# Kernel optimization log

Measured on AMD Instinct MI355X. Metric: run time of the kernel, lower is better.

## Reference

```python
import jax, jax.numpy as jnp
import numpy as np

NUM_HEADS = 8
NEG_INF = float(-2**32 + 1)
LN_EPS = 1e-8


def setup_inputs() -> dict:
    key = jax.random.key(0)
    ks = jax.random.split(key, 9)
    B, T, D = 4, 2048, 512
    inp = {
        "queries": jax.random.normal(ks[0], (B, T, D), jnp.float32),
        "keys": jax.random.normal(ks[1], (B, T, D), jnp.float32),
        "values": jax.random.normal(ks[2], (B, T, D), jnp.float32),
        "Wq": jax.random.normal(ks[3], (D, D), jnp.float32) / np.sqrt(D),
        "bq": jnp.zeros((D,), jnp.float32),
        "Wk": jax.random.normal(ks[4], (D, D), jnp.float32) / np.sqrt(D),
        "bk": jnp.zeros((D,), jnp.float32),
        "Wv": jax.random.normal(ks[5], (D, D), jnp.float32) / np.sqrt(D),
        "bv": jnp.zeros((D,), jnp.float32),
        "gamma": jnp.ones((D,), jnp.float32),
        "beta": jnp.zeros((D,), jnp.float32),
    }
    return inp


def _split_heads(x, h):
    # torch.cat(torch.chunk(x, h, dim=2), dim=0): [B,T,D] -> [h*B, T, D/h], head-major
    B, T, D = x.shape
    return x.reshape(B, T, h, D // h).transpose(2, 0, 1, 3).reshape(h * B, T, D // h)


def _merge_heads(x, h, B):
    # inverse: [h*B, T, dh] -> [B, T, h*dh]
    hB, T, dh = x.shape
    return x.reshape(h, B, T, dh).transpose(1, 2, 0, 3).reshape(B, T, h * dh)


def reference(queries, keys, values, Wq, bq, Wk, bk, Wv, bv, gamma, beta):
    h = NUM_HEADS
    B, Tq, D = queries.shape
    dh = D // h

    Q = jax.nn.relu(queries @ Wq + bq)
    K = jax.nn.relu(keys @ Wk + bk)
    V = jax.nn.relu(values @ Wv + bv)

    Q_ = _split_heads(Q, h)  # [h*B, Tq, dh]
    K_ = _split_heads(K, h)
    V_ = _split_heads(V, h)

    scores = jnp.einsum('bqd,bkd->bqk', Q_, K_) / jnp.sqrt(jnp.float32(dh))  # [h*B, Tq, Tk]

    # key padding mask: zero rows in `keys` get -inf scores
    key_mask = jnp.sign(jnp.abs(jnp.sum(keys, axis=-1)))  # [B, Tk]
    key_mask = jnp.tile(key_mask, (h, 1))  # [h*B, Tk]
    scores = jnp.where(key_mask[:, None, :] == 0.0, NEG_INF, scores)

    attn = jax.nn.softmax(scores, axis=-1)

    # query mask applied multiplicatively post-softmax
    query_mask = jnp.sign(jnp.abs(jnp.sum(queries, axis=-1)))  # [B, Tq]
    query_mask = jnp.tile(query_mask, (h, 1))  # [h*B, Tq]
    attn = attn * query_mask[:, :, None]

    out = jnp.einsum('bqk,bkd->bqd', attn, V_)  # [h*B, Tq, dh]
    out = _merge_heads(out, h, B) + queries  # residual

    # custom LayerNorm: torch.std is unbiased (ddof=1), eps added to std
    mean = out.mean(-1, keepdims=True)
    std = jnp.sqrt(out.var(-1, ddof=1, keepdims=True))
    return gamma * (out - mean) / (std + LN_EPS) + beta
```

## Files before the change

### kernel.cpp

```cpp
#include <hip/hip_runtime.h>


typedef __attribute__((ext_vector_type(8))) __bf16 bf16x8;
typedef __attribute__((ext_vector_type(4))) float f32x4;

#if __has_builtin(__builtin_amdgcn_exp2f)
#define EXP2F __builtin_amdgcn_exp2f
#else
#define EXP2F exp2f
#endif

#define QSCALE (0.125f * 1.4426950408889634f)

__device__ __forceinline__ unsigned short f2bf(float f) {
  return __builtin_bit_cast(unsigned short, (__bf16)f);
}
__device__ __forceinline__ unsigned pk2(float a, float b) {
  return (unsigned)f2bf(a) | ((unsigned)f2bf(b) << 16);
}
__device__ __forceinline__ f32x4 mfma16(bf16x8 a, bf16x8 b, f32x4 c) {
  return __builtin_amdgcn_mfma_f32_16x16x32_bf16(a, b, c, 0, 0, 0);
}
__device__ __forceinline__ bf16x8 ld_bf8(const unsigned short* p) {
  return *(const bf16x8*)p;
}
__device__ __forceinline__ void g2l16(const void* g, void* l) {
  __builtin_amdgcn_global_load_lds(
      (const __attribute__((address_space(1))) void*)g,
      (__attribute__((address_space(3))) void*)l, 16, 0, 0);
}

__global__ __launch_bounds__(256) void wt_kernel(const float* __restrict__ Wq,
                                                 const float* __restrict__ Wk,
                                                 const float* __restrict__ Wv,
                                                 unsigned short* __restrict__ Wt) {
  int idx = blockIdx.x * 256 + threadIdx.x;
  int o = idx * 8;
  int z = o >> 18;
  int rem = o & 262143;
  int n = rem >> 9;
  int k0 = rem & 511;
  const float* W = (z == 0) ? Wq : ((z == 1) ? Wk : Wv);
  unsigned int w[4];
#pragma unroll
  for (int i = 0; i < 4; ++i) {
    unsigned short lo = f2bf(W[(k0 + 2 * i) * 512 + n]);
    unsigned short hi = f2bf(W[(k0 + 2 * i + 1) * 512 + n]);
    w[i] = (unsigned)lo | ((unsigned)hi << 16);
  }
  *(uint4*)(Wt + o) = make_uint4(w[0], w[1], w[2], w[3]);
}

__global__ __launch_bounds__(256) void xcvt_kernel(
    const float* __restrict__ Xq, const float* __restrict__ Xk,
    const float* __restrict__ Xv, unsigned short* __restrict__ Xbq,
    unsigned short* __restrict__ Xbk, unsigned short* __restrict__ Xbv,
    float* __restrict__ qmask, float* __restrict__ kbias) {
  int row = blockIdx.x * 4 + (threadIdx.x >> 6);
  int lane = threadIdx.x & 63;
  int z = row >> 13;
  int r = row & 8191;
  const float* X = (z == 0) ? Xq : ((z == 1) ? Xk : Xv);
  unsigned short* Xb = (z == 0) ? Xbq : ((z == 1) ? Xbk : Xbv);
  const float* p = X + r * 512 + lane * 8;
  f32x4 lo = *(const f32x4*)p;
  f32x4 hi = *(const f32x4*)(p + 4);
  *(uint4*)(Xb + r * 512 + lane * 8) =
      make_uint4(pk2(lo[0], lo[1]), pk2(lo[2], lo[3]), pk2(hi[0], hi[1]),
                 pk2(hi[2], hi[3]));
  if (z < 2) {
    float s = lo[0] + lo[1] + lo[2] + lo[3] + hi[0] + hi[1] + hi[2] + hi[3];
#pragma unroll
    for (int off = 1; off < 64; off <<= 1) s += __shfl_xor(s, off);
    if (lane == 0) {
      if (z == 0)
        qmask[r] = (s == 0.f) ? 0.f : 1.f;
      else
        kbias[r] = (s == 0.f) ? -1.0e30f : 0.f;
    }
  }
}

__global__ __launch_bounds__(256, 3) void proj_kernel(
    const unsigned short* __restrict__ Xbq, const unsigned short* __restrict__ Xbk,
    const unsigned short* __restrict__ Xbv, const float* __restrict__ bq,
    const float* __restrict__ bk, const float* __restrict__ bv,
    const unsigned short* __restrict__ Wt, unsigned short* __restrict__ Qb,
    unsigned short* __restrict__ Kb, unsigned short* __restrict__ Vt) {
  __shared__ unsigned short Asm[2][128][32];
  __shared__ unsigned short Bsm[2][128][32];

  int tid = threadIdx.x;
  int m0g = blockIdx.x * 128;
  int z = m0g >> 13;
  int m0 = m0g & 8191;
  int n0 = blockIdx.y * 128;
  const unsigned short* Xb = (z == 0) ? Xbq : ((z == 1) ? Xbk : Xbv);
  const float* bias = (z == 0) ? bq : ((z == 1) ? bk : bv);
  const unsigned short* Wz = Wt + z * 262144;

  int w = tid >> 6, lane = tid & 63;
  int wm = w >> 1, wn = w & 1;
  int mrow = lane & 15, quad = lane >> 4;

  int srow = tid >> 2, sslot = tid & 3;
  int sxs = sslot ^ ((srow >> 1) & 3);
  const unsigned short* gA = Xb + (m0 + srow) * 512 + sxs * 8;
  const unsigned short* gB = Wz + (n0 + srow) * 512 + sxs * 8;
  char* lA = (char*)&Asm[0][0][0] + tid * 16;
  char* lB = (char*)&Bsm[0][0][0] + tid * 16;

  int rs = (quad ^ ((mrow >> 1) & 3)) * 8;

  f32x4 zero = {0.f, 0.f, 0.f, 0.f};
  f32x4 acc[4][4];
#pragma unroll
  for (int i = 0; i < 4; ++i)
#pragma unroll
    for (int j = 0; j < 4; ++j) acc[i][j] = zero;

  g2l16(gA, lA);
  g2l16(gA + 64 * 512, lA + 4096);
  g2l16(gB, lB);
  g2l16(gB + 64 * 512, lB + 4096);
  __syncthreads();

  for (int kc = 0; kc < 16; ++kc) {
    int cur = kc & 1;
    if (kc < 15) {
      int ko = (kc + 1) * 32;
      int nb = cur ^ 1;
      g2l16(gA + ko, lA + nb * 8192);
      g2l16(gA + ko + 64 * 512, lA + nb * 8192 + 4096);
      g2l16(gB + ko, lB + nb * 8192);
      g2l16(gB + ko + 64 * 512, lB + nb * 8192 + 4096);
    }
    bf16x8 af[4], bfr[4];
#pragma unroll
    for (int mt = 0; mt < 4; ++mt)
      af[mt] = ld_bf8(&Asm[cur][wm * 64 + mt * 16 + mrow][rs]);
#pragma unroll
    for (int nt = 0; nt < 4; ++nt)
      bfr[nt] = ld_bf8(&Bsm[cur][wn * 64 + nt * 16 + mrow][rs]);
#pragma unroll
    for (int mt = 0; mt < 4; ++mt)
#pragma unroll
      for (int nt = 0; nt < 4; ++nt)
        acc[mt][nt] = mfma16(af[mt], bfr[nt], acc[mt][nt]);
    __syncthreads();
  }

  if (z < 2) {
    unsigned short* dst = (z == 0) ? Qb : Kb;
    float sc = (z == 0) ? QSCALE : 1.0f;
#pragma unroll
    for (int nt = 0; nt < 4; ++nt) {
      int n = n0 + wn * 64 + nt * 16 + mrow;
      float bv_ = bias[n];
#pragma unroll
      for (int mt = 0; mt < 4; ++mt) {
        int m = m0 + wm * 64 + mt * 16 + quad * 4;
#pragma unroll
        for (int r = 0; r < 4; ++r) {
          float v = fmaxf(acc[mt][nt][r] + bv_, 0.f) * sc;
          dst[(m + r) * 512 + n] = f2bf(v);
        }
      }
    }
  } else {
#pragma unroll
    for (int nt = 0; nt < 4; ++nt) {
      int n = n0 + wn * 64 + nt * 16 + mrow;
      int hh = n >> 6, jj = n & 63;
      float bv_ = bias[n];
#pragma unroll
      for (int mt = 0; mt < 4; ++mt) {
        int grow = m0 + wm * 64 + mt * 16 + quad * 4;
        int bb = grow >> 11, tl = grow & 2047;
        int pos = (tl & ~31) + quad * 8 + (mt & 1) * 4;
        float p0 = fmaxf(acc[mt][nt][0] + bv_, 0.f);
        float p1 = fmaxf(acc[mt][nt][1] + bv_, 0.f);
        float p2 = fmaxf(acc[mt][nt][2] + bv_, 0.f);
        float p3 = fmaxf(acc[mt][nt][3] + bv_, 0.f);
        *(uint2*)(Vt + ((hh * 4 + bb) * 64 + jj) * 2048 + pos) =
            make_uint2(pk2(p0, p1), pk2(p2, p3));
      }
    }
  }
}

__global__ __launch_bounds__(256, 2) void attn_kernel(
    const unsigned short* __restrict__ Qb, const unsigned short* __restrict__ Kb,
    const unsigned short* __restrict__ Vt, const float* __restrict__ qmask,
    const float* __restrict__ kbias, const float* __restrict__ queries,
    float* __restrict__ out) {
  __shared__ char smem[65536];
  unsigned short* KsmS = (unsigned short*)smem;
  unsigned short* VsmS = (unsigned short*)(smem + 32768);

  int hb = blockIdx.x;
  int qt = blockIdx.y;
  int h = hb >> 2, b = hb & 3;
  int q0 = qt * 128;
  int tid = threadIdx.x;
  int w = tid >> 6, lane = tid & 63;
  int mrow = lane & 15, quad = lane >> 4;
  int mlow = mrow & 7;

  const unsigned short* gK =
      Kb + (b * 2048 + (tid >> 3)) * 512 + h * 64 + (((tid & 7) ^ ((tid >> 3) & 7)) * 8);
  const unsigned short* gV =
      Vt + (hb * 64 + (tid >> 4)) * 2048 + (((tid & 15) ^ ((tid >> 4) & 15)) * 8);

  bf16x8 qf[2][2];
  {
    const unsigned short* qp =
        Qb + (b * 2048 + q0 + w * 32 + mrow) * 512 + h * 64 + quad * 8;
#pragma unroll
    for (int qn = 0; qn < 2; ++qn) {
      qf[qn][0] = ld_bf8(qp + qn * 8192);
      qf[qn][1] = ld_bf8(qp + qn * 8192 + 32);
    }
  }

  bf16x8 onev;
#pragma unroll
  for (int i = 0; i < 8; ++i) onev[i] = (__bf16)1.0f;

  f32x4 zero = {0.f, 0.f, 0.f, 0.f};
  f32x4 oacc[4][2];
#pragma unroll
  for (int i = 0; i < 4; ++i)
#pragma unroll
    for (int j = 0; j < 2; ++j) oacc[i][j] = zero;
  f32x4 lacc[2] = {zero, zero};

  const float* kmB = kbias + b * 2048 + quad * 4;

#pragma unroll
  for (int j = 0; j < 4; ++j) {
    g2l16(gK + j * 32 * 512, &KsmS[j * 2048 + tid * 8]);
    g2l16(gV + j * 16 * 2048, &VsmS[j * 2048 + tid * 8]);
  }

  for (int it = 0; it < 16; ++it) {
    int bi = it & 1;
    int kb = it * 128;
    __syncthreads();

    if (it < 15) {
      int nb = 1 - bi;
      int nkb = kb + 128;
#pragma unroll
      for (int j = 0; j < 4; ++j) {
        g2l16(gK + (nkb + j * 32) * 512, &KsmS[nb * 8192 + j * 2048 + tid * 8]);
        g2l16(gV + nkb + j * 16 * 2048, &VsmS[nb * 8192 + j * 2048 + tid * 8]);
      }
    }

    const unsigned short* Kc = KsmS + bi * 8192;
    const unsigned short* Vc = VsmS + bi * 8192;

    bf16x8 kf[2][4], vf[2][4];
    f32x4 km[2][2];
    auto ldg = [&](int gi, int sl) {
      km[sl][0] = *(const f32x4*)(kmB + kb + gi * 32);
      km[sl][1] = *(const f32x4*)(kmB + kb + gi * 32 + 16);
      kf[sl][0] = ld_bf8(&Kc[(gi * 32 + mrow) * 64 + (quad ^ mlow) * 8]);
      kf[sl][1] = ld_bf8(&Kc[(gi * 32 + mrow) * 64 + ((4 + quad) ^ mlow) * 8]);
      kf[sl][2] = ld_bf8(&Kc[(gi * 32 + 16 + mrow) * 64 + (quad ^ mlow) * 8]);
      kf[sl][3] = ld_bf8(&Kc[(gi * 32 + 16 + mrow) * 64 + ((4 + quad) ^ mlow) * 8]);
#pragma unroll
      for (int dt = 0; dt < 4; ++dt)
        vf[sl][dt] =
            ld_bf8(&Vc[(dt * 16 + mrow) * 128 + ((gi * 4 + quad) ^ mrow) * 8]);
    };

    ldg(0, 0);
#pragma unroll
    for (int g = 0; g < 4; ++g) {
      int cb = g & 1;
      if (g < 3) ldg(g + 1, cb ^ 1);
#pragma unroll
      for (int qn = 0; qn < 2; ++qn) {
        f32x4 s0 = mfma16(kf[cb][0], qf[qn][0], km[cb][0]);
        s0 = mfma16(kf[cb][1], qf[qn][1], s0);
        f32x4 s1 = mfma16(kf[cb][2], qf[qn][0], km[cb][1]);
        s1 = mfma16(kf[cb][3], qf[qn][1], s1);
        f32x4 p0, p1;
#pragma unroll
        for (int r = 0; r < 4; ++r) {
          p0[r] = EXP2F(s0[r]);
          p1[r] = EXP2F(s1[r]);
        }
        bf16x8 pf = __builtin_bit_cast(
            bf16x8, make_uint4(pk2(p0[0], p0[1]), pk2(p0[2], p0[3]),
                               pk2(p1[0], p1[1]), pk2(p1[2], p1[3])));
        lacc[qn] = mfma16(pf, onev, lacc[qn]);
#pragma unroll
        for (int dt = 0; dt < 4; ++dt)
          oacc[dt][qn] = mfma16(pf, vf[cb][dt], oacc[dt][qn]);
      }
    }
  }

#pragma unroll
  for (int qn = 0; qn < 2; ++qn) {
#pragma unroll
    for (int r = 0; r < 4; ++r) {
      int qg = b * 2048 + q0 + w * 32 + qn * 16 + quad * 4 + r;
      float inv = qmask[qg] / lacc[qn][r];
      const float* qsrc = queries + qg * 512 + h * 64 + mrow;
      float* od = out + qg * 512 + h * 64 + mrow;
#pragma unroll
      for (int dt = 0; dt < 4; ++dt)
        od[dt * 16] = oacc[dt][qn][r] * inv + qsrc[dt * 16];
    }
  }
}

__global__ __launch_bounds__(256) void ln_kernel(float* __restrict__ out,
                                                 const float* __restrict__ gamma,
                                                 const float* __restrict__ beta) {
  int row = blockIdx.x * 4 + (threadIdx.x >> 6);
  int lane = threadIdx.x & 63;
  float* p = out + row * 512;
  float4 v1 = ((const float4*)p)[lane];
  float4 v2 = ((const float4*)p)[64 + lane];
  float s = v1.x + v1.y + v1.z + v1.w + v2.x + v2.y + v2.z + v2.w;
  float sq = v1.x * v1.x + v1.y * v1.y + v1.z * v1.z + v1.w * v1.w +
             v2.x * v2.x + v2.y * v2.y + v2.z * v2.z + v2.w * v2.w;
#pragma unroll
  for (int off = 32; off > 0; off >>= 1) {
    s += __shfl_xor(s, off);
    sq += __shfl_xor(sq, off);
  }
  float mean = s * (1.f / 512.f);
  float var = fmaxf((sq - 512.f * mean * mean) * (1.f / 511.f), 0.f);
  float inv = 1.f / (sqrtf(var) + 1e-8f);
  float4 g1 = ((const float4*)gamma)[lane];
  float4 g2 = ((const float4*)gamma)[64 + lane];
  float4 b1 = ((const float4*)beta)[lane];
  float4 b2 = ((const float4*)beta)[64 + lane];
  v1.x = g1.x * (v1.x - mean) * inv + b1.x;
  v1.y = g1.y * (v1.y - mean) * inv + b1.y;
  v1.z = g1.z * (v1.z - mean) * inv + b1.z;
  v1.w = g1.w * (v1.w - mean) * inv + b1.w;
  v2.x = g2.x * (v2.x - mean) * inv + b2.x;
  v2.y = g2.y * (v2.y - mean) * inv + b2.y;
  v2.z = g2.z * (v2.z - mean) * inv + b2.z;
  v2.w = g2.w * (v2.w - mean) * inv + b2.w;
  ((float4*)p)[lane] = v1;
  ((float4*)p)[64 + lane] = v2;
}

extern "C" void kernel_launch(void* const* d_in, const int* in_sizes, int n_in,
                              void* d_out, int out_size, void* d_ws, size_t ws_size,
                              hipStream_t stream) {
  (void)in_sizes; (void)n_in; (void)out_size; (void)ws_size;
  const float* queries = (const float*)d_in[0];
  const float* keys    = (const float*)d_in[1];
  const float* values  = (const float*)d_in[2];
  const float* Wq = (const float*)d_in[3];
  const float* bq = (const float*)d_in[4];
  const float* Wk = (const float*)d_in[5];
  const float* bk = (const float*)d_in[6];
  const float* Wv = (const float*)d_in[7];
  const float* bv = (const float*)d_in[8];
  const float* gamma = (const float*)d_in[9];
  const float* beta  = (const float*)d_in[10];
  float* out = (float*)d_out;

  char* ws = (char*)d_ws;
  unsigned short* Qb = (unsigned short*)(ws);
  unsigned short* Kb = (unsigned short*)(ws + 8 * 1024 * 1024);
  unsigned short* Vt = (unsigned short*)(ws + 16 * 1024 * 1024);
  unsigned short* Wt = (unsigned short*)(ws + 24 * 1024 * 1024);
  unsigned short* Xbv = (unsigned short*)(ws + 26 * 1024 * 1024);
  float* qmask = (float*)(ws + 34 * 1024 * 1024);
  float* kbias = qmask + 8192;

  unsigned short* Xbq = (unsigned short*)d_out;
  unsigned short* Xbk = Xbq + 4194304;

  wt_kernel<<<384, 256, 0, stream>>>(Wq, Wk, Wv, Wt);
  xcvt_kernel<<<6144, 256, 0, stream>>>(queries, keys, values, Xbq, Xbk, Xbv,
                                        qmask, kbias);
  proj_kernel<<<dim3(192, 4), 256, 0, stream>>>(Xbq, Xbk, Xbv, bq, bk, bv,
                                                Wt, Qb, Kb, Vt);
  attn_kernel<<<dim3(32, 16), 256, 0, stream>>>(Qb, Kb, Vt, qmask, kbias,
                                                queries, out);
  ln_kernel<<<2048, 256, 0, stream>>>(out, gamma, beta);
}
```

Measured before the change: 187.2 us.

## Split attention over the key dimension and merge partial sums in the layernorm kernel

```diff
diff --git a/kernel.cpp b/kernel.cpp
--- a/kernel.cpp
+++ b/kernel.cpp
@@ -189,38 +189,38 @@
   }
 }
 
-__global__ __launch_bounds__(256, 2) void attn_kernel(
+__global__ __launch_bounds__(256, 4) void attn_kernel(
     const unsigned short* __restrict__ Qb, const unsigned short* __restrict__ Kb,
-    const unsigned short* __restrict__ Vt, const float* __restrict__ qmask,
-    const float* __restrict__ kbias, const float* __restrict__ queries,
-    float* __restrict__ out) {
-  __shared__ char smem[65536];
+    const unsigned short* __restrict__ Vt, const float* __restrict__ kbias,
+    float* __restrict__ O0, float* __restrict__ O1,
+    float* __restrict__ l0, float* __restrict__ l1) {
+  __shared__ char smem[32768];
   unsigned short* KsmS = (unsigned short*)smem;
-  unsigned short* VsmS = (unsigned short*)(smem + 32768);
 
   int hb = blockIdx.x;
   int qt = blockIdx.y;
+  int z = blockIdx.z;
   int h = hb >> 2, b = hb & 3;
   int q0 = qt * 128;
+  int k0 = z * 1024;
   int tid = threadIdx.x;
   int w = tid >> 6, lane = tid & 63;
   int mrow = lane & 15, quad = lane >> 4;
   int mlow = mrow & 7;
 
   const unsigned short* gK =
-      Kb + (b * 2048 + (tid >> 3)) * 512 + h * 64 + (((tid & 7) ^ ((tid >> 3) & 7)) * 8);
-  const unsigned short* gV =
-      Vt + (hb * 64 + (tid >> 4)) * 2048 + (((tid & 15) ^ ((tid >> 4) & 15)) * 8);
+      Kb + (b * 2048 + k0 + (tid >> 3)) * 512 + h * 64 +
+      (((tid & 7) ^ ((tid >> 3) & 7)) * 8);
+  const unsigned short* gVb = Vt + (hb * 64 + mrow) * 2048 + k0;
 
   bf16x8 qf[2][2];
   {
     const unsigned short* qp =
         Qb + (b * 2048 + q0 + w * 32 + mrow) * 512 + h * 64 + quad * 8;
-#pragma unroll
-    for (int qn = 0; qn < 2; ++qn) {
-      qf[qn][0] = ld_bf8(qp + qn * 8192);
-      qf[qn][1] = ld_bf8(qp + qn * 8192 + 32);
-    }
+    qf[0][0] = ld_bf8(qp);
+    qf[0][1] = ld_bf8(qp + 32);
+    qf[1][0] = ld_bf8(qp + 8192);
+    qf[1][1] = ld_bf8(qp + 8192 + 32);
   }
 
   bf16x8 onev;
@@ -235,45 +235,38 @@
     for (int j = 0; j < 2; ++j) oacc[i][j] = zero;
   f32x4 lacc[2] = {zero, zero};
 
-  const float* kmB = kbias + b * 2048 + quad * 4;
-
-#pragma unroll
-  for (int j = 0; j < 4; ++j) {
+  const float* kmC = kbias + b * 2048 + k0 + quad * 4;
+
+#pragma unroll
+  for (int j = 0; j < 4; ++j)
     g2l16(gK + j * 32 * 512, &KsmS[j * 2048 + tid * 8]);
-    g2l16(gV + j * 16 * 2048, &VsmS[j * 2048 + tid * 8]);
-  }
-
-  for (int it = 0; it < 16; ++it) {
+
+  for (int it = 0; it < 8; ++it) {
     int bi = it & 1;
     int kb = it * 128;
     __syncthreads();
 
-    if (it < 15) {
+    if (it < 7) {
       int nb = 1 - bi;
-      int nkb = kb + 128;
-#pragma unroll
-      for (int j = 0; j < 4; ++j) {
-        g2l16(gK + (nkb + j * 32) * 512, &KsmS[nb * 8192 + j * 2048 + tid * 8]);
-        g2l16(gV + nkb + j * 16 * 2048, &VsmS[nb * 8192 + j * 2048 + tid * 8]);
-      }
+#pragma unroll
+      for (int j = 0; j < 4; ++j)
+        g2l16(gK + (kb + 128 + j * 32) * 512, &KsmS[nb * 8192 + j * 2048 + tid * 8]);
     }
 
     const unsigned short* Kc = KsmS + bi * 8192;
-    const unsigned short* Vc = VsmS + bi * 8192;
 
     bf16x8 kf[2][4], vf[2][4];
     f32x4 km[2][2];
     auto ldg = [&](int gi, int sl) {
-      km[sl][0] = *(const f32x4*)(kmB + kb + gi * 32);
-      km[sl][1] = *(const f32x4*)(kmB + kb + gi * 32 + 16);
+      km[sl][0] = *(const f32x4*)(kmC + kb + gi * 32);
+      km[sl][1] = *(const f32x4*)(kmC + kb + gi * 32 + 16);
       kf[sl][0] = ld_bf8(&Kc[(gi * 32 + mrow) * 64 + (quad ^ mlow) * 8]);
       kf[sl][1] = ld_bf8(&Kc[(gi * 32 + mrow) * 64 + ((4 + quad) ^ mlow) * 8]);
       kf[sl][2] = ld_bf8(&Kc[(gi * 32 + 16 + mrow) * 64 + (quad ^ mlow) * 8]);
       kf[sl][3] = ld_bf8(&Kc[(gi * 32 + 16 + mrow) * 64 + ((4 + quad) ^ mlow) * 8]);
 #pragma unroll
       for (int dt = 0; dt < 4; ++dt)
-        vf[sl][dt] =
-            ld_bf8(&Vc[(dt * 16 + mrow) * 128 + ((gi * 4 + quad) ^ mrow) * 8]);
+        vf[sl][dt] = ld_bf8(gVb + dt * 32768 + kb + (gi * 4 + quad) * 8);
     };
 
     ldg(0, 0);
@@ -281,6 +274,7 @@
     for (int g = 0; g < 4; ++g) {
       int cb = g & 1;
       if (g < 3) ldg(g + 1, cb ^ 1);
+      __builtin_amdgcn_s_setprio(1);
 #pragma unroll
       for (int qn = 0; qn < 2; ++qn) {
         f32x4 s0 = mfma16(kf[cb][0], qf[qn][0], km[cb][0]);
@@ -301,32 +295,56 @@
         for (int dt = 0; dt < 4; ++dt)
           oacc[dt][qn] = mfma16(pf, vf[cb][dt], oacc[dt][qn]);
       }
-    }
-  }
-
+      __builtin_amdgcn_s_setprio(0);
+    }
+  }
+
+  float* Op = z ? O1 : O0;
+  float* lp = (z ? l1 : l0) + h * 8192;
 #pragma unroll
   for (int qn = 0; qn < 2; ++qn) {
 #pragma unroll
     for (int r = 0; r < 4; ++r) {
       int qg = b * 2048 + q0 + w * 32 + qn * 16 + quad * 4 + r;
-      float inv = qmask[qg] / lacc[qn][r];
-      const float* qsrc = queries + qg * 512 + h * 64 + mrow;
-      float* od = out + qg * 512 + h * 64 + mrow;
+      if (mrow == 0) lp[qg] = lacc[qn][r];
+      float* od = Op + qg * 512 + h * 64 + mrow;
 #pragma unroll
       for (int dt = 0; dt < 4; ++dt)
-        od[dt * 16] = oacc[dt][qn][r] * inv + qsrc[dt * 16];
-    }
-  }
-}
-
-__global__ __launch_bounds__(256) void ln_kernel(float* __restrict__ out,
-                                                 const float* __restrict__ gamma,
-                                                 const float* __restrict__ beta) {
+        od[dt * 16] = oacc[dt][qn][r];
+    }
+  }
+}
+
+__global__ __launch_bounds__(256) void ln_kernel(
+    float* __restrict__ out, const float* __restrict__ O1,
+    const float* __restrict__ l0, const float* __restrict__ l1,
+    const float* __restrict__ qmask, const float* __restrict__ queries,
+    const float* __restrict__ gamma, const float* __restrict__ beta) {
   int row = blockIdx.x * 4 + (threadIdx.x >> 6);
   int lane = threadIdx.x & 63;
+  int h1 = lane >> 4;
+  int h2 = 4 + h1;
+  float qm = qmask[row];
+  float sa = qm / (l0[h1 * 8192 + row] + l1[h1 * 8192 + row]);
+  float sb = qm / (l0[h2 * 8192 + row] + l1[h2 * 8192 + row]);
   float* p = out + row * 512;
-  float4 v1 = ((const float4*)p)[lane];
-  float4 v2 = ((const float4*)p)[64 + lane];
+  const float4* p1v = (const float4*)(O1 + row * 512);
+  const float4* pq = (const float4*)(queries + row * 512);
+  float4 a1 = ((const float4*)p)[lane];
+  float4 a2 = ((const float4*)p)[64 + lane];
+  float4 o1 = p1v[lane];
+  float4 o2 = p1v[64 + lane];
+  float4 q1 = pq[lane];
+  float4 q2 = pq[64 + lane];
+  float4 v1, v2;
+  v1.x = (a1.x + o1.x) * sa + q1.x;
+  v1.y = (a1.y + o1.y) * sa + q1.y;
+  v1.z = (a1.z + o1.z) * sa + q1.z;
+  v1.w = (a1.w + o1.w) * sa + q1.w;
+  v2.x = (a2.x + o2.x) * sb + q2.x;
+  v2.y = (a2.y + o2.y) * sb + q2.y;
+  v2.z = (a2.z + o2.z) * sb + q2.z;
+  v2.w = (a2.w + o2.w) * sb + q2.w;
   float s = v1.x + v1.y + v1.z + v1.w + v2.x + v2.y + v2.z + v2.w;
   float sq = v1.x * v1.x + v1.y * v1.y + v1.z * v1.z + v1.w * v1.w +
              v2.x * v2.x + v2.y * v2.y + v2.z * v2.z + v2.w * v2.w;
@@ -377,18 +395,23 @@
   unsigned short* Vt = (unsigned short*)(ws + 16 * 1024 * 1024);
   unsigned short* Wt = (unsigned short*)(ws + 24 * 1024 * 1024);
   unsigned short* Xbv = (unsigned short*)(ws + 26 * 1024 * 1024);
-  float* qmask = (float*)(ws + 34 * 1024 * 1024);
+  float* O1 = (float*)(ws + 24 * 1024 * 1024);
+  float* qmask = (float*)(ws + 40 * 1024 * 1024);
   float* kbias = qmask + 8192;
+  float* l0 = kbias + 8192;
+  float* l1 = l0 + 65536;
 
   unsigned short* Xbq = (unsigned short*)d_out;
   unsigned short* Xbk = Xbq + 4194304;
+  float* O0 = (float*)d_out;
 
   wt_kernel<<<384, 256, 0, stream>>>(Wq, Wk, Wv, Wt);
   xcvt_kernel<<<6144, 256, 0, stream>>>(queries, keys, values, Xbq, Xbk, Xbv,
                                         qmask, kbias);
   proj_kernel<<<dim3(192, 4), 256, 0, stream>>>(Xbq, Xbk, Xbv, bq, bk, bv,
                                                 Wt, Qb, Kb, Vt);
-  attn_kernel<<<dim3(32, 16), 256, 0, stream>>>(Qb, Kb, Vt, qmask, kbias,
-                                                queries, out);
-  ln_kernel<<<2048, 256, 0, stream>>>(out, gamma, beta);
-}
+  attn_kernel<<<dim3(32, 16, 2), 256, 0, stream>>>(Qb, Kb, Vt, kbias,
+                                                   O0, O1, l0, l1);
+  ln_kernel<<<2048, 256, 0, stream>>>(out, O1, l0, l1, qmask, queries,
+                                      gamma, beta);
+}
```

New measurement: 403.3 us. 2.15x slower.

## Merge weight transpose into input conversion and software-pipeline QK scores in attention

Applied to the files above, without the earlier changes.

```diff
diff --git a/kernel.cpp b/kernel.cpp
--- a/kernel.cpp
+++ b/kernel.cpp
@@ -30,53 +30,66 @@
       (__attribute__((address_space(3))) void*)l, 16, 0, 0);
 }
 
-__global__ __launch_bounds__(256) void wt_kernel(const float* __restrict__ Wq,
-                                                 const float* __restrict__ Wk,
-                                                 const float* __restrict__ Wv,
-                                                 unsigned short* __restrict__ Wt) {
-  int idx = blockIdx.x * 256 + threadIdx.x;
-  int o = idx * 8;
-  int z = o >> 18;
-  int rem = o & 262143;
-  int n = rem >> 9;
-  int k0 = rem & 511;
-  const float* W = (z == 0) ? Wq : ((z == 1) ? Wk : Wv);
-  unsigned int w[4];
-#pragma unroll
-  for (int i = 0; i < 4; ++i) {
-    unsigned short lo = f2bf(W[(k0 + 2 * i) * 512 + n]);
-    unsigned short hi = f2bf(W[(k0 + 2 * i + 1) * 512 + n]);
-    w[i] = (unsigned)lo | ((unsigned)hi << 16);
-  }
-  *(uint4*)(Wt + o) = make_uint4(w[0], w[1], w[2], w[3]);
-}
-
-__global__ __launch_bounds__(256) void xcvt_kernel(
+__global__ __launch_bounds__(256) void prep_kernel(
     const float* __restrict__ Xq, const float* __restrict__ Xk,
-    const float* __restrict__ Xv, unsigned short* __restrict__ Xbq,
-    unsigned short* __restrict__ Xbk, unsigned short* __restrict__ Xbv,
+    const float* __restrict__ Xv, const float* __restrict__ Wq,
+    const float* __restrict__ Wk, const float* __restrict__ Wv,
+    unsigned short* __restrict__ Xbq, unsigned short* __restrict__ Xbk,
+    unsigned short* __restrict__ Xbv, unsigned short* __restrict__ Wt,
     float* __restrict__ qmask, float* __restrict__ kbias) {
-  int row = blockIdx.x * 4 + (threadIdx.x >> 6);
-  int lane = threadIdx.x & 63;
-  int z = row >> 13;
-  int r = row & 8191;
-  const float* X = (z == 0) ? Xq : ((z == 1) ? Xk : Xv);
-  unsigned short* Xb = (z == 0) ? Xbq : ((z == 1) ? Xbk : Xbv);
-  const float* p = X + r * 512 + lane * 8;
-  f32x4 lo = *(const f32x4*)p;
-  f32x4 hi = *(const f32x4*)(p + 4);
-  *(uint4*)(Xb + r * 512 + lane * 8) =
-      make_uint4(pk2(lo[0], lo[1]), pk2(lo[2], lo[3]), pk2(hi[0], hi[1]),
-                 pk2(hi[2], hi[3]));
-  if (z < 2) {
-    float s = lo[0] + lo[1] + lo[2] + lo[3] + hi[0] + hi[1] + hi[2] + hi[3];
-#pragma unroll
-    for (int off = 1; off < 64; off <<= 1) s += __shfl_xor(s, off);
-    if (lane == 0) {
-      if (z == 0)
-        qmask[r] = (s == 0.f) ? 0.f : 1.f;
-      else
-        kbias[r] = (s == 0.f) ? -1.0e30f : 0.f;
+  __shared__ float T[64][65];
+  int tid = threadIdx.x;
+  if (blockIdx.x < 6144) {
+    int row = blockIdx.x * 4 + (tid >> 6);
+    int lane = tid & 63;
+    int z = row >> 13;
+    int r = row & 8191;
+    const float* X = (z == 0) ? Xq : ((z == 1) ? Xk : Xv);
+    unsigned short* Xb = (z == 0) ? Xbq : ((z == 1) ? Xbk : Xbv);
+    const float* p = X + r * 512 + lane * 8;
+    f32x4 lo = *(const f32x4*)p;
+    f32x4 hi = *(const f32x4*)(p + 4);
+    *(uint4*)(Xb + r * 512 + lane * 8) =
+        make_uint4(pk2(lo[0], lo[1]), pk2(lo[2], lo[3]), pk2(hi[0], hi[1]),
+                   pk2(hi[2], hi[3]));
+    if (z < 2) {
+      float s = lo[0] + lo[1] + lo[2] + lo[3] + hi[0] + hi[1] + hi[2] + hi[3];
+#pragma unroll
+      for (int off = 1; off < 64; off <<= 1) s += __shfl_xor(s, off);
+      if (lane == 0) {
+        if (z == 0)
+          qmask[r] = (s == 0.f) ? 0.f : 1.f;
+        else
+          kbias[r] = (s == 0.f) ? -1.0e30f : 0.f;
+      }
+    }
+  } else {
+    int bid = blockIdx.x - 6144;
+    int z = bid >> 6;
+    int t = bid & 63;
+    int r0 = (t >> 3) * 64;
+    int c0 = (t & 7) * 64;
+    const float* W = (z == 0) ? Wq : ((z == 1) ? Wk : Wv);
+    int tr = tid >> 4, tc = tid & 15;
+#pragma unroll
+    for (int j = 0; j < 4; ++j) {
+      int row = r0 + tr + j * 16;
+      float4 v = *(const float4*)&W[row * 512 + c0 + tc * 4];
+      T[tc * 4 + 0][tr + j * 16] = v.x;
+      T[tc * 4 + 1][tr + j * 16] = v.y;
+      T[tc * 4 + 2][tr + j * 16] = v.z;
+      T[tc * 4 + 3][tr + j * 16] = v.w;
+    }
+    __syncthreads();
+    unsigned short* Wz = Wt + z * 262144;
+#pragma unroll
+    for (int j = 0; j < 4; ++j) {
+      int nl = tr + j * 16;
+      int kl = tc * 4;
+      float a0 = T[nl][kl], a1 = T[nl][kl + 1];
+      float a2 = T[nl][kl + 2], a3 = T[nl][kl + 3];
+      *(uint2*)(Wz + (c0 + nl) * 512 + r0 + kl) =
+          make_uint2(pk2(a0, a1), pk2(a2, a3));
     }
   }
 }
@@ -216,11 +229,10 @@
   {
     const unsigned short* qp =
         Qb + (b * 2048 + q0 + w * 32 + mrow) * 512 + h * 64 + quad * 8;
-#pragma unroll
-    for (int qn = 0; qn < 2; ++qn) {
-      qf[qn][0] = ld_bf8(qp + qn * 8192);
-      qf[qn][1] = ld_bf8(qp + qn * 8192 + 32);
-    }
+    qf[0][0] = ld_bf8(qp);
+    qf[0][1] = ld_bf8(qp + 32);
+    qf[1][0] = ld_bf8(qp + 8192);
+    qf[1][1] = ld_bf8(qp + 8192 + 32);
   }
 
   bf16x8 onev;
@@ -262,36 +274,50 @@
     const unsigned short* Vc = VsmS + bi * 8192;
 
     bf16x8 kf[2][4], vf[2][4];
-    f32x4 km[2][2];
-    auto ldg = [&](int gi, int sl) {
+    f32x4 km[2][2], sA[2][2], sB[2][2];
+
+    auto ldK = [&](int gi, int sl) {
       km[sl][0] = *(const f32x4*)(kmB + kb + gi * 32);
       km[sl][1] = *(const f32x4*)(kmB + kb + gi * 32 + 16);
       kf[sl][0] = ld_bf8(&Kc[(gi * 32 + mrow) * 64 + (quad ^ mlow) * 8]);
       kf[sl][1] = ld_bf8(&Kc[(gi * 32 + mrow) * 64 + ((4 + quad) ^ mlow) * 8]);
       kf[sl][2] = ld_bf8(&Kc[(gi * 32 + 16 + mrow) * 64 + (quad ^ mlow) * 8]);
       kf[sl][3] = ld_bf8(&Kc[(gi * 32 + 16 + mrow) * 64 + ((4 + quad) ^ mlow) * 8]);
+    };
+    auto ldV = [&](int gi, int sl) {
 #pragma unroll
       for (int dt = 0; dt < 4; ++dt)
         vf[sl][dt] =
             ld_bf8(&Vc[(dt * 16 + mrow) * 128 + ((gi * 4 + quad) ^ mrow) * 8]);
     };
-
-    ldg(0, 0);
+    auto doS = [&](int sl) {
+#pragma unroll
+      for (int qn = 0; qn < 2; ++qn) {
+        f32x4 t0 = mfma16(kf[sl][0], qf[qn][0], km[sl][0]);
+        sA[sl][qn] = mfma16(kf[sl][1], qf[qn][1], t0);
+        f32x4 t1 = mfma16(kf[sl][2], qf[qn][0], km[sl][1]);
+        sB[sl][qn] = mfma16(kf[sl][3], qf[qn][1], t1);
+      }
+    };
+
+    ldK(0, 0);
+    ldV(0, 0);
+    ldK(1, 1);
+    doS(0);
 #pragma unroll
     for (int g = 0; g < 4; ++g) {
-      int cb = g & 1;
-      if (g < 3) ldg(g + 1, cb ^ 1);
+      int cs = g & 1, ns = cs ^ 1;
+      if (g < 2) ldK(g + 2, cs);
+      if (g < 3) ldV(g + 1, ns);
+      __builtin_amdgcn_s_setprio(1);
+      if (g < 3) doS(ns);
 #pragma unroll
       for (int qn = 0; qn < 2; ++qn) {
-        f32x4 s0 = mfma16(kf[cb][0], qf[qn][0], km[cb][0]);
-        s0 = mfma16(kf[cb][1], qf[qn][1], s0);
-        f32x4 s1 = mfma16(kf[cb][2], qf[qn][0], km[cb][1]);
-        s1 = mfma16(kf[cb][3], qf[qn][1], s1);
         f32x4 p0, p1;
 #pragma unroll
         for (int r = 0; r < 4; ++r) {
-          p0[r] = EXP2F(s0[r]);
-          p1[r] = EXP2F(s1[r]);
+          p0[r] = EXP2F(sA[cs][qn][r]);
+          p1[r] = EXP2F(sB[cs][qn][r]);
         }
         bf16x8 pf = __builtin_bit_cast(
             bf16x8, make_uint4(pk2(p0[0], p0[1]), pk2(p0[2], p0[3]),
@@ -299,8 +325,9 @@
         lacc[qn] = mfma16(pf, onev, lacc[qn]);
 #pragma unroll
         for (int dt = 0; dt < 4; ++dt)
-          oacc[dt][qn] = mfma16(pf, vf[cb][dt], oacc[dt][qn]);
-      }
+          oacc[dt][qn] = mfma16(pf, vf[cs][dt], oacc[dt][qn]);
+      }
+      __builtin_amdgcn_s_setprio(0);
     }
   }
 
@@ -383,9 +410,8 @@
   unsigned short* Xbq = (unsigned short*)d_out;
   unsigned short* Xbk = Xbq + 4194304;
 
-  wt_kernel<<<384, 256, 0, stream>>>(Wq, Wk, Wv, Wt);
-  xcvt_kernel<<<6144, 256, 0, stream>>>(queries, keys, values, Xbq, Xbk, Xbv,
-                                        qmask, kbias);
+  prep_kernel<<<6336, 256, 0, stream>>>(queries, keys, values, Wq, Wk, Wv,
+                                        Xbq, Xbk, Xbv, Wt, qmask, kbias);
   proj_kernel<<<dim3(192, 4), 256, 0, stream>>>(Xbq, Xbk, Xbv, bq, bk, bv,
                                                 Wt, Qb, Kb, Vt);
   attn_kernel<<<dim3(32, 16), 256, 0, stream>>>(Qb, Kb, Vt, qmask, kbias,
```

Measured after the change: 177.1 us. 1.06x faster.
